# Optimization experiments

Measured on AMD Instinct MI355X. Metric: run time of the kernel, lower is better.

The kernel has to match this reference:

```python
import jax, jax.numpy as jnp
import numpy as np

V, D, F, H, NB, S, B = 16384, 512, 2048, 8, 4, 512, 2
T_STEPS = 3      # config.T: number of PC inference iterations
GAMMA = 0.1      # state-update step size


def _layernorm(x, s, b):
    m = x.mean(-1, keepdims=True)
    v = ((x - m) ** 2).mean(-1, keepdims=True)
    return (x - m) * jax.lax.rsqrt(v + 1e-5) * s + b


def setup_inputs() -> dict:
    key = jax.random.key(0)
    ks = jax.random.split(key, 12)
    r = lambda k, sh: jax.random.normal(k, sh, jnp.float32) * 0.02
    return {
        'word_emb': r(ks[0], (V, D)),
        'pos_emb': r(ks[1], (S, D)),
        'Wq': r(ks[2], (NB, D, D)),
        'Wk': r(ks[3], (NB, D, D)),
        'Wv': r(ks[4], (NB, D, D)),
        'bq': jnp.zeros((NB, D), jnp.float32),
        'bk': jnp.zeros((NB, D), jnp.float32),
        'bv': jnp.zeros((NB, D), jnp.float32),
        'Wo': r(ks[5], (NB, D, D)),
        'bo': jnp.zeros((NB, D), jnp.float32),
        'ln1_s': jnp.ones((NB, D), jnp.float32),
        'ln1_b': jnp.zeros((NB, D), jnp.float32),
        'ln2_s': jnp.ones((NB, D), jnp.float32),
        'ln2_b': jnp.zeros((NB, D), jnp.float32),
        'W1': r(ks[6], (NB, D, F)),
        'b1': jnp.zeros((NB, F), jnp.float32),
        'W2': r(ks[7], (NB, F, D)),
        'b2': jnp.zeros((NB, D), jnp.float32),
        'Wout': r(ks[8], (D, V)),
        'bout': jnp.zeros((V,), jnp.float32),
        'input_ids': jax.random.randint(ks[9], (B, S), 0, V),
        'target_ids': jax.random.randint(ks[10], (B, S), 0, V),
    }


def _forward(word_emb, pos_emb, Wq, Wk, Wv, bq, bk, bv, Wo, bo,
             ln1_s, ln1_b, ln2_s, ln2_b, W1, b1, W2, b2, Wout, bout,
             input_ids, target_ids):
    Bsz, Sl = input_ids.shape
    dh = D // H
    scale = 1.0 / float(np.sqrt(dh))
    ids = jnp.clip(input_ids, 0, V - 1)
    target = jax.nn.one_hot(jnp.clip(target_ids, 0, V - 1), V, dtype=word_emb.dtype)
    # bottom prediction: word + position embeddings
    mu_emb = word_emb[ids] + pos_emb[jnp.arange(Sl)][None]  # (B,S,D)
    causal = jnp.tril(jnp.ones((Sl, Sl), bool))
    neg = jnp.finfo(word_emb.dtype).min

    def attn(x, b):
        h = _layernorm(x, ln1_s[b], ln1_b[b])
        q = (h @ Wq[b] + bq[b]).reshape(Bsz, Sl, H, dh)
        k = (h @ Wk[b] + bk[b]).reshape(Bsz, Sl, H, dh)
        v = (h @ Wv[b] + bv[b]).reshape(Bsz, Sl, H, dh)
        sc = jnp.einsum('bqhd,bkhd->bhqk', q, k) * scale
        sc = jnp.where(causal, sc, neg)
        a = jax.nn.softmax(sc, axis=-1)
        return jnp.einsum('bhqk,bkhd->bqhd', a, v).reshape(Bsz, Sl, D)

    # generative functions g[l]: x_l -> mu_{l+1}; 4 PC layers per block
    # (pc_qkv->attn ctx, pc_output->Wo, pc_layer1->gelu(fc1), pc_layer2->fc2)
    gs = []
    for b in range(NB):
        gs.append(lambda x, b=b: attn(x, b))
        gs.append(lambda x, b=b: x @ Wo[b] + bo[b])
        gs.append(lambda x, b=b: jax.nn.gelu(_layernorm(x, ln2_s[b], ln2_b[b]) @ W1[b] + b1[b]))
        gs.append(lambda x, b=b: x @ W2[b] + b2[b])
    g_top = lambda x: x @ Wout + bout  # output pc layer -> logits mu

    # init_x: forward sweep sets each latent to its prediction
    xs = [mu_emb]
    for g in gs:
        xs.append(g(xs[-1]))
    L = len(gs)

    # T-step iterative PC inference: eps_l = x_l - mu_l, top clamped to target
    # x_l <- x_l + GAMMA * (J_{g_l}(x_l)^T eps_{l+1} - eps_l)
    for _ in range(T_STEPS):
        preds, vjps = [], []
        for l in range(L):
            mu, vj = jax.vjp(gs[l], xs[l])
            preds.append(mu)
            vjps.append(vj)
        logits, vj_top = jax.vjp(g_top, xs[L])
        eps = [xs[0] - mu_emb] + [xs[l + 1] - preds[l] for l in range(L)]
        eps_top = logits - target
        new_xs = []
        for l in range(L + 1):
            td = vjps[l](eps[l + 1])[0] if l < L else vj_top(eps_top)[0]
            new_xs.append(xs[l] + GAMMA * (td - eps[l]))
        xs = new_xs

    return g_top(xs[L])  # get_mu('linear_output')


def reference(word_emb, pos_emb, Wq, Wk, Wv, bq, bk, bv, Wo, bo,
              ln1_s, ln1_b, ln2_s, ln2_b, W1, b1, W2, b2, Wout, bout,
              input_ids, target_ids):
    return _forward(word_emb, pos_emb, Wq, Wk, Wv, bq, bk, bv, Wo, bo,
                    ln1_s, ln1_b, ln2_s, ln2_b, W1, b1, W2, b2, Wout, bout,
                    input_ids, target_ids)
```

## Files before the change

kernel.cpp:

```cpp
#include <hip/hip_runtime.h>
#include <hip/hip_bf16.h>
#include <math.h>

#define D_   512
#define F_   2048
#define V_   16384
#define H_   8
#define DH_  64
#define S_   512
#define B_   2
#define M_   1024
#define MD_  (M_ * D_)
#define MF_  (M_ * F_)
#define GAMMA_ 0.1f

typedef unsigned int u32;
typedef unsigned short u16;
typedef __attribute__((ext_vector_type(4))) float f32x4;
typedef __attribute__((ext_vector_type(8))) short s16x8;
typedef __attribute__((ext_vector_type(4))) u16 u16x4;
typedef __attribute__((ext_vector_type(8))) u16 u16x8;

__device__ __forceinline__ u16 f2b(float f) {
    __hip_bfloat16 h = __float2bfloat16(f);
    return *reinterpret_cast<u16*>(&h);
}
__device__ __forceinline__ float b2f(u16 v) {
    u32 u = ((u32)v) << 16;
    float f; __builtin_memcpy(&f, &u, 4); return f;
}
__device__ __forceinline__ u16x4 pack4(f32x4 v) {
    u16x4 o; o.x = f2b(v[0]); o.y = f2b(v[1]); o.z = f2b(v[2]); o.w = f2b(v[3]);
    return o;
}

__device__ __forceinline__ void gl_lds16(const void* g, void* l) {
    __builtin_amdgcn_global_load_lds((const __attribute__((address_space(1))) u32*)g,
                                     (__attribute__((address_space(3))) u32*)l, 16, 0, 0);
}

__device__ __forceinline__ float gelu_f(float v) {
    float u = 0.7978845608028654f * (v + 0.044715f * v * v * v);
    return 0.5f * v * (1.f + tanhf(u));
}

__device__ __forceinline__ f32x4 xpose4(f32x4 v, int b) {
#pragma unroll
    for (int s = 1; s < 4; s <<= 1) {
        f32x4 nv;
#pragma unroll
        for (int j = 0; j < 4; ++j) {
            float ex = __shfl_xor(v[j ^ s], s, 64);
            nv[j] = ((b ^ j) & s) ? ex : v[j];
        }
        v = nv;
    }
    return v;
}

__device__ __forceinline__ float wave_sum(float v) {
#pragma unroll
    for (int o = 32; o > 0; o >>= 1) v += __shfl_xor(v, o, 64);
    return v;
}

#define E_F32   0
#define E_GELU  1
#define E_TD    2
#define E_EC2   3
#define E_QKV3  4
#define E_OUT   5
#define E_BF16  6
#define E_SYM   7

template<int BK>
__device__ __forceinline__ int swz(int c, int row) {
    if constexpr (BK == 32) return c ^ ((row >> 1) & 3);
    else                    return c ^ (row & 7);
}

template<int BM, int BN, int BK, int FM, int FN, int EPI>
__global__ __launch_bounds__(256)
void mfma_gemm(const u16* __restrict__ A, const u16* __restrict__ B,
               float* __restrict__ Cf, u16* __restrict__ Cb,
               u16* __restrict__ Cb2, u16* __restrict__ Cb3,
               const float* __restrict__ bias,
               int K, int lda, int ldb, int ldc,
               long sC, long sKz, float alpha,
               const float* __restrict__ base, const float* __restrict__ subv,
               const float* __restrict__ cvec, const u16* __restrict__ woutTb,
               const int* __restrict__ tcl,
               float* __restrict__ ebF, u16* __restrict__ ebB)
{
    constexpr int WC = BN / (FN * 16);
    static_assert((BM / (FM * 16)) * WC == 4, "4 waves");
    constexpr int LPR = BK / 8;
    constexpr int RPI = 2048 / BK;
    constexpr int NISS = BM / RPI + BN / RPI;
    if constexpr (EPI == E_SYM) {
        if (blockIdx.x > blockIdx.y) return;
    }
    __shared__ __align__(16) u16 Asl[3][BM * BK];
    __shared__ __align__(16) u16 Bsl[3][BN * BK];
    const int t = threadIdx.x, l = t & 63, wid = t >> 6;
    const int m0 = blockIdx.y * BM, n0 = blockIdx.x * BN;
    const long z = blockIdx.z;
    A += z * sKz;
    B += z * sKz;
    if (Cf) Cf += z * sC;

    f32x4 acc[FM][FN] = {};
    const int rm = (wid / WC) * (FM * 16), cn = (wid % WC) * (FN * 16);
    const int lr = l & 15, hi = l >> 4;
    const int srl = t / LPR, sc = t % LPR;

    auto stage = [&](int k0, int pb) {
#pragma unroll
        for (int i = 0; i < BM / RPI; ++i) {
            int row = i * RPI + srl;
            gl_lds16(A + (size_t)(m0 + row) * lda + k0 + swz<BK>(sc, row) * 8,
                     &Asl[pb][i * 2048 + t * 8]);
        }
#pragma unroll
        for (int i = 0; i < BN / RPI; ++i) {
            int row = i * RPI + srl;
            gl_lds16(B + (size_t)(n0 + row) * ldb + k0 + swz<BK>(sc, row) * 8,
                     &Bsl[pb][i * 2048 + t * 8]);
        }
    };
    auto compute = [&](int pb) {
#pragma unroll
        for (int kk = 0; kk < BK / 32; ++kk) {
            s16x8 av[FM], bv[FN];
#pragma unroll
            for (int fm = 0; fm < FM; ++fm)
                av[fm] = *(const s16x8*)&Asl[pb][(rm + fm * 16 + lr) * BK + swz<BK>(kk * 4 + hi, lr) * 8];
#pragma unroll
            for (int fn = 0; fn < FN; ++fn)
                bv[fn] = *(const s16x8*)&Bsl[pb][(cn + fn * 16 + lr) * BK + swz<BK>(kk * 4 + hi, lr) * 8];
#pragma unroll
            for (int fm = 0; fm < FM; ++fm)
#pragma unroll
                for (int fn = 0; fn < FN; ++fn)
                    acc[fm][fn] = __builtin_amdgcn_mfma_f32_16x16x32_bf16(av[fm], bv[fn], acc[fm][fn], 0, 0, 0);
        }
    };

    const int nst = K / BK;
    stage(0, 0);
    if (nst > 1) stage(BK, 1);
    int rd = 0, wr = 2;
    for (int s = 0; s < nst; ++s) {
        if (s < nst - 1)
            asm volatile("s_waitcnt vmcnt(%0)" :: "i"(NISS) : "memory");
        else
            asm volatile("s_waitcnt vmcnt(0)" ::: "memory");
        __builtin_amdgcn_s_barrier();
        __builtin_amdgcn_sched_barrier(0);
        compute(rd);
        if (s + 2 < nst) stage((s + 2) * BK, wr);
        rd = (rd + 1 == 3) ? 0 : rd + 1;
        wr = (wr + 1 == 3) ? 0 : wr + 1;
    }

    const int qb = lr & 3, qi = lr >> 2;
#pragma unroll
    for (int fm = 0; fm < FM; ++fm)
#pragma unroll
        for (int fn = 0; fn < FN; ++fn) {
            const int gm = m0 + rm + fm * 16 + hi * 4 + qb;
            const int gn0 = n0 + cn + fn * 16 + qi * 4;
            const size_t idx0 = (size_t)gm * ldc + gn0;
            if constexpr (EPI == E_QKV3) {
                const int gnf = n0 + cn + fn * 16;
                const int sel = gnf >> 9;
                if (sel < 2) {
                    f32x4 v = xpose4(acc[fm][fn], qb);
                    f32x4 bv4 = *(const f32x4*)&bias[gn0];
#pragma unroll
                    for (int j = 0; j < 4; ++j) v[j] += bv4[j];
                    int b = gm >> 9, s = gm & (S_ - 1);
                    int d9 = gn0 & 511, h = d9 >> 6, d = d9 & 63;
                    u16* dst = (sel == 0) ? Cb : Cb2;
                    *(u16x4*)&dst[(((size_t)(b * H_ + h) * S_ + s) << 6) + d] = pack4(v);
                } else {
                    const int gnl = gnf + lr;
                    const int gm0 = m0 + rm + fm * 16 + hi * 4;
                    int b = gm0 >> 9, s0 = gm0 & (S_ - 1);
                    int d9 = gnl & 511, h = d9 >> 6, d = d9 & 63;
                    float bb = bias[gnl];
                    f32x4 v = acc[fm][fn];
#pragma unroll
                    for (int j = 0; j < 4; ++j) v[j] += bb;
                    *(u16x4*)&Cb3[((((size_t)(b * H_ + h)) << 6) + d) * S_ + s0] = pack4(v);
                }
            } else if constexpr (EPI == E_SYM) {
                const int gnr = n0 + cn + fn * 16 + lr;
                const int mc0 = m0 + rm + fm * 16 + hi * 4;
                *(f32x4*)&Cf[(size_t)gnr * ldc + mc0] = acc[fm][fn];
                f32x4 v = xpose4(acc[fm][fn], qb);
                *(f32x4*)&Cf[idx0] = v;
            } else {
                f32x4 v = xpose4(acc[fm][fn], qb);
                if constexpr (EPI == E_F32) {
#pragma unroll
                    for (int j = 0; j < 4; ++j) v[j] *= alpha;
                    if (bias) {
                        f32x4 bv4 = *(const f32x4*)&bias[gn0];
#pragma unroll
                        for (int j = 0; j < 4; ++j) v[j] += bv4[j];
                    }
                    *(f32x4*)&Cf[idx0] = v;
                    if (Cb) *(u16x4*)&Cb[idx0] = pack4(v);
                } else if constexpr (EPI == E_OUT) {
                    f32x4 bv4 = *(const f32x4*)&bias[gn0];
#pragma unroll
                    for (int j = 0; j < 4; ++j) v[j] += bv4[j];
                    *(f32x4*)&Cf[idx0] = v;
                } else if constexpr (EPI == E_GELU) {
                    f32x4 bv4 = *(const f32x4*)&bias[gn0];
#pragma unroll
                    for (int j = 0; j < 4; ++j) v[j] = gelu_f(v[j] + bv4[j]);
                    *(u16x4*)&Cb[idx0] = pack4(v);
                } else if constexpr (EPI == E_TD) {
                    const int tc = tcl[gm];
                    f32x4 cv4 = *(const f32x4*)&cvec[gn0];
                    f32x4 ba4 = *(const f32x4*)&base[idx0];
                    u16x4 gv = *(const u16x4*)&woutTb[(size_t)tc * D_ + gn0];
                    f32x4 dlt, o2;
#pragma unroll
                    for (int j = 0; j < 4; ++j)
                        dlt[j] = GAMMA_ * (v[j] + cv4[j] - b2f(gv[j]));
                    if (subv) {
                        f32x4 sv4 = *(const f32x4*)&subv[idx0];
#pragma unroll
                        for (int j = 0; j < 4; ++j) dlt[j] -= GAMMA_ * sv4[j];
                    }
#pragma unroll
                    for (int j = 0; j < 4; ++j) o2[j] = ba4[j] + dlt[j];
                    if (Cf) *(f32x4*)&Cf[idx0] = o2;
                    *(u16x4*)&Cb[idx0] = pack4(o2);
                    if (ebF) *(f32x4*)&ebF[idx0] = dlt;
                    if (ebB) *(u16x4*)&ebB[idx0] = pack4(dlt);
                } else if constexpr (EPI == E_EC2) {
                    f32x4 ba4 = *(const f32x4*)&base[idx0];
                    f32x4 sv4 = *(const f32x4*)&subv[idx0];
#pragma unroll
                    for (int j = 0; j < 4; ++j) v[j] = ba4[j] - sv4[j] - GAMMA_ * v[j];
                    *(f32x4*)&Cf[idx0] = v;
                } else if constexpr (EPI == E_BF16) {
                    *(u16x4*)&Cb[idx0] = pack4(v);
                }
            }
        }
}

__global__ __launch_bounds__(128)
void flash_attn(const u16* __restrict__ q, const u16* __restrict__ k,
                const u16* __restrict__ vT, u16* __restrict__ ctx)
{
    __shared__ __align__(16) u16 Ks[3][64 * 64];
    __shared__ __align__(16) u16 Vs[3][64 * 64];
    __shared__ __align__(16) u16 Ps[2][16 * 64];
    const int t = threadIdx.x, l = t & 63, w = t >> 6;
    const int qt = blockIdx.x, z = blockIdx.y;
    const int bb = z >> 3, hh = z & 7;
    const int lr = l & 15, hi = l >> 4;
    const u16* qp = q + (((size_t)z * S_ + qt * 32 + w * 16) << 6);
    const u16* kp = k + ((size_t)z * S_ << 6);
    const u16* vp = vT + (((size_t)z) << 6) * S_;

    const s16x8 aq0 = *(const s16x8*)&qp[lr * 64 + hi * 8];
    const s16x8 aq1 = *(const s16x8*)&qp[lr * 64 + 32 + hi * 8];

    f32x4 o[4] = {};
    float m[4], ls[4];
#pragma unroll
    for (int r = 0; r < 4; ++r) { m[r] = -3.0e38f; ls[r] = 0.f; }
    const int qrow = qt * 32 + w * 16 + hi * 4;
    const int srow = t >> 3, scl = t & 7;
    const int cg = (scl ^ (srow & 7)) * 8;
    const int sw7 = (lr & 7);
    const int jmax = qt >> 1;

    auto stage = [&](int j, int pb) {
#pragma unroll
        for (int i = 0; i < 4; ++i)
            gl_lds16(kp + ((size_t)(j * 64 + i * 16 + srow) << 6) + cg,
                     &Ks[pb][i * 1024 + t * 8]);
#pragma unroll
        for (int i = 0; i < 4; ++i)
            gl_lds16(vp + (size_t)(i * 16 + srow) * S_ + j * 64 + cg,
                     &Vs[pb][i * 1024 + t * 8]);
    };

    stage(0, 0);
    if (jmax > 0) stage(1, 1);
    int rd = 0, wr = 2;
    for (int j = 0; j <= jmax; ++j) {
        if (j < jmax) asm volatile("s_waitcnt vmcnt(8)" ::: "memory");
        else          asm volatile("s_waitcnt vmcnt(0)" ::: "memory");
        __builtin_amdgcn_s_barrier();
        __builtin_amdgcn_sched_barrier(0);

        float pv[4][4];
        __builtin_amdgcn_s_setprio(1);
#pragma unroll
        for (int fn = 0; fn < 4; ++fn) {
            f32x4 acc = {};
            acc = __builtin_amdgcn_mfma_f32_16x16x32_bf16(aq0,
                    *(const s16x8*)&Ks[rd][((fn * 16 + lr) << 6) + ((hi ^ sw7) * 8)], acc, 0, 0, 0);
            acc = __builtin_amdgcn_mfma_f32_16x16x32_bf16(aq1,
                    *(const s16x8*)&Ks[rd][((fn * 16 + lr) << 6) + (((hi + 4) ^ sw7) * 8)], acc, 0, 0, 0);
#pragma unroll
            for (int r = 0; r < 4; ++r) pv[fn][r] = acc[r] * 0.125f;
        }
        __builtin_amdgcn_s_setprio(0);
        if (j == jmax) {
#pragma unroll
            for (int fn = 0; fn < 4; ++fn) {
                int col = j * 64 + fn * 16 + lr;
#pragma unroll
                for (int r = 0; r < 4; ++r)
                    if (col > qrow + r) pv[fn][r] = -3.0e38f;
            }
        }
        float sc[4], rs[4];
#pragma unroll
        for (int r = 0; r < 4; ++r) {
            float x = fmaxf(fmaxf(pv[0][r], pv[1][r]), fmaxf(pv[2][r], pv[3][r]));
#pragma unroll
            for (int off = 1; off < 16; off <<= 1) x = fmaxf(x, __shfl_xor(x, off, 64));
            float nm = fmaxf(m[r], x);
            sc[r] = expf(m[r] - nm);
            m[r] = nm;
            rs[r] = 0.f;
        }
#pragma unroll
        for (int fn = 0; fn < 4; ++fn)
#pragma unroll
            for (int r = 0; r < 4; ++r) {
                float p = expf(pv[fn][r] - m[r]);
                pv[fn][r] = p;
                rs[r] += p;
            }
#pragma unroll
        for (int r = 0; r < 4; ++r) {
#pragma unroll
            for (int off = 1; off < 16; off <<= 1) rs[r] += __shfl_xor(rs[r], off, 64);
            ls[r] = ls[r] * sc[r] + rs[r];
        }
#pragma unroll
        for (int fn = 0; fn < 4; ++fn)
#pragma unroll
            for (int r = 0; r < 4; ++r) o[fn][r] *= sc[r];
#pragma unroll
        for (int fn = 0; fn < 4; ++fn)
#pragma unroll
            for (int r = 0; r < 4; ++r) {
                int qr = hi * 4 + r;
                int ci = (2 * fn + (lr >> 3)) ^ (qr & 7);
                Ps[w][qr * 64 + ci * 8 + (lr & 7)] = f2b(pv[fn][r]);
            }
        __builtin_amdgcn_s_setprio(1);
#pragma unroll
        for (int ks = 0; ks < 2; ++ks) {
            const s16x8 pa = *(const s16x8*)&Ps[w][lr * 64 + (((4 * ks + hi) ^ sw7) * 8)];
#pragma unroll
            for (int fn = 0; fn < 4; ++fn)
                o[fn] = __builtin_amdgcn_mfma_f32_16x16x32_bf16(pa,
                        *(const s16x8*)&Vs[rd][((fn * 16 + lr) << 6) + (((hi + 4 * ks) ^ sw7) * 8)], o[fn], 0, 0, 0);
        }
        __builtin_amdgcn_s_setprio(0);
        if (j + 2 <= jmax) stage(j + 2, wr);
        rd = (rd + 1 == 3) ? 0 : rd + 1;
        wr = (wr + 1 == 3) ? 0 : wr + 1;
    }
    float inv[4];
#pragma unroll
    for (int r = 0; r < 4; ++r) inv[r] = 1.f / ls[r];
    u16* cp = ctx + ((size_t)(bb * S_ + qt * 32 + w * 16) * D_) + hh * 64;
    const int qb = lr & 3, qi = lr >> 2;
#pragma unroll
    for (int fn = 0; fn < 4; ++fn) {
        f32x4 v = o[fn];
#pragma unroll
        for (int r = 0; r < 4; ++r) v[r] *= inv[r];
        v = xpose4(v, qb);
        *(u16x4*)&cp[(size_t)(hi * 4 + qb) * D_ + fn * 16 + qi * 4] = pack4(v);
    }
}

__global__ __launch_bounds__(256)
void mega_prep(const float* __restrict__ Wq, const float* __restrict__ Wk,
               const float* __restrict__ Wv, const float* __restrict__ Wo,
               const float* __restrict__ W1, const float* __restrict__ W2,
               const float* __restrict__ Wout,
               const float* __restrict__ bq, const float* __restrict__ bk,
               const float* __restrict__ bv, const int* __restrict__ target_ids,
               const float* __restrict__ we, const float* __restrict__ pe,
               const int* __restrict__ input_ids,
               const float* __restrict__ ln1s0, const float* __restrict__ ln1b0,
               u16* __restrict__ wqkvT, u16* __restrict__ woT, u16* __restrict__ w1T,
               u16* __restrict__ w2T, u16* __restrict__ woutT,
               u16* __restrict__ woutD, float* __restrict__ qkvb, int* __restrict__ tcl,
               u16* __restrict__ h_b)
{
    __shared__ float tile[64][65];
    __shared__ float sh2[4];
    const int g = blockIdx.x, t = threadIdx.x;

    if (g >= 1281) {
        const int rr = (g - 1281) * 2 + (t >> 7);
        const int lc = t & 127;
        const int ss = rr & (S_ - 1);
        int id = input_ids[rr];
        id = id < 0 ? 0 : (id > V_ - 1 ? V_ - 1 : id);
        const float4 a = ((const float4*)we)[(size_t)id * 128 + lc];
        const float4 b = ((const float4*)pe)[(size_t)ss * 128 + lc];
        float4 x;
        x.x = a.x + b.x; x.y = a.y + b.y; x.z = a.z + b.z; x.w = a.w + b.w;
        const int w = t >> 6, wb = (t >> 7) << 1;
        float s = wave_sum(x.x + x.y + x.z + x.w);
        if ((t & 63) == 0) sh2[w] = s;
        __syncthreads();
        float mu = (sh2[wb] + sh2[wb + 1]) * (1.f / D_);
        float d0 = x.x - mu, d1 = x.y - mu, d2 = x.z - mu, d3 = x.w - mu;
        float qv = wave_sum(d0 * d0 + d1 * d1 + d2 * d2 + d3 * d3);
        __syncthreads();
        if ((t & 63) == 0) sh2[w] = qv;
        __syncthreads();
        float var = (sh2[wb] + sh2[wb + 1]) * (1.f / D_);
        float r = rsqrtf(var + 1e-5f);
        const int c0 = lc * 4;
        float4 scv = *(const float4*)&ln1s0[c0];
        float4 bbv = *(const float4*)&ln1b0[c0];
        f32x4 o;
        o[0] = d0 * r * scv.x + bbv.x; o[1] = d1 * r * scv.y + bbv.y;
        o[2] = d2 * r * scv.z + bbv.z; o[3] = d3 * r * scv.w + bbv.w;
        *(u16x4*)&h_b[(size_t)rr * D_ + c0] = pack4(o);
        return;
    }
    if (g == 1280) {
        for (int i = t; i < M_; i += 256) {
            int v = target_ids[i];
            tcl[i] = v < 0 ? 0 : (v > V_ - 1 ? V_ - 1 : v);
        }
        for (int i = t; i < 4 * 1536; i += 256) {
            int b = i / 1536, j = i - b * 1536;
            qkvb[i] = (j < 512) ? bq[b * 512 + j]
                    : (j < 1024) ? bk[b * 512 + j - 512] : bv[b * 512 + j - 1024];
        }
        return;
    }

    const float* in = nullptr;
    u16 *outT = nullptr, *outC = nullptr;
    int R = 512, C = 512, c0 = 0, rbase = 0;

    if (g < 192) {
        int sel = g / 64, rem = g % 64, zz = rem >> 4, st = (rem >> 1) & 7, hf = rem & 1;
        in = (sel == 0 ? Wq : sel == 1 ? Wk : Wv) + (size_t)zz * 262144;
        outT = wqkvT + (size_t)zz * 786432 + sel * 262144;
        c0 = st * 64; rbase = hf * 256;
    } else if (g < 256) {
        int rem = g - 192, zz = rem >> 4, st = (rem >> 1) & 7, hf = rem & 1;
        in = Wo + (size_t)zz * 262144; outT = woT + (size_t)zz * 262144;
        c0 = st * 64; rbase = hf * 256;
    } else if (g < 512) {
        int rem = g - 256, zz = rem >> 6, sub = rem & 63, st = sub >> 1, hf = sub & 1;
        in = W1 + (size_t)zz * 1048576; outT = w1T + (size_t)zz * 1048576;
        C = 2048; c0 = st * 64; rbase = hf * 256;
    } else if (g < 768) {
        int rem = g - 512, zz = rem >> 6, sub = rem & 63, st = sub & 7, ch = sub >> 3;
        in = W2 + (size_t)zz * 1048576; outT = w2T + (size_t)zz * 1048576;
        R = 2048; c0 = st * 64; rbase = ch * 256;
    } else {
        int rem = g - 768, st = rem >> 1, hf = rem & 1;
        in = Wout; outT = woutT; outC = woutD;
        C = 16384; c0 = st * 64; rbase = hf * 256;
    }

    const int lrow = t >> 4, lcol = (t & 15) * 4;
    float4 va[2][4];
    auto loadit = [&](int it, int pb) {
#pragma unroll
        for (int p = 0; p < 4; ++p)
            va[pb][p] = *(const float4*)&in[(size_t)(rbase + it * 64 + p * 16 + lrow) * C + c0 + lcol];
    };

    loadit(0, 0);
#pragma unroll
    for (int it = 0; it < 4; ++it) {
        const int cur = it & 1;
        const int r0 = rbase + it * 64;
#pragma unroll
        for (int p = 0; p < 4; ++p) {
            float4 v = va[cur][p];
            int row = p * 16 + lrow;
            tile[row][lcol] = v.x; tile[row][lcol + 1] = v.y;
            tile[row][lcol + 2] = v.z; tile[row][lcol + 3] = v.w;
            if (outC) {
                f32x4 fv; fv[0] = v.x; fv[1] = v.y; fv[2] = v.z; fv[3] = v.w;
                *(u16x4*)&outC[(size_t)(r0 + row) * C + c0 + lcol] = pack4(fv);
            }
        }
        __syncthreads();
        if (it < 3) loadit(it + 1, cur ^ 1);
#pragma unroll
        for (int p = 0; p < 2; ++p) {
            int orow = p * 32 + (t >> 3), oc = (t & 7) * 8;
            u16x8 o;
#pragma unroll
            for (int j = 0; j < 8; ++j) o[j] = f2b(tile[oc + j][orow]);
            *(u16x8*)&outT[(size_t)(c0 + orow) * R + r0 + oc] = o;
        }
        __syncthreads();
    }
}

__global__ __launch_bounds__(256)
void gredcvec(const float* __restrict__ P, u16* __restrict__ G,
              const u16* __restrict__ woutD, const float* __restrict__ bout,
              float* __restrict__ cvec, const u16* __restrict__ w2T3,
              u16* __restrict__ H2)
{
    __shared__ __align__(16) u16 As2[2][32 * 64];
    __shared__ __align__(16) u16 Bs2[2][64 * 64];
    const int blk = blockIdx.x, t = threadIdx.x;
    if (blk < 1024) {
        int i = blk * 256 + t;
        float s = 0.f;
#pragma unroll
        for (int zz = 0; zz < 16; ++zz) s += P[(size_t)zz * D_ * D_ + i];
        G[i] = f2b(s);
    } else if (blk < 1152) {
        const int w = t >> 6, l = t & 63;
        const int d = (blk - 1024) * 4 + w;
        float s = 0.f;
        for (int it = 0; it < 32; ++it) {
            int base = it * 512 + l * 8;
            u16x8 wv = *(const u16x8*)&woutD[(size_t)d * V_ + base];
            float4 b0 = *(const float4*)&bout[base];
            float4 b1 = *(const float4*)&bout[base + 4];
            s += b2f(wv[0]) * b0.x + b2f(wv[1]) * b0.y + b2f(wv[2]) * b0.z + b2f(wv[3]) * b0.w
               + b2f(wv[4]) * b1.x + b2f(wv[5]) * b1.y + b2f(wv[6]) * b1.z + b2f(wv[7]) * b1.w;
        }
        s = wave_sum(s);
        if (l == 0) cvec[d] = s;
    } else {
        const int idx = blk - 1152;
        const int n0 = (idx & 7) * 64, m0 = (idx >> 3) * 32;
        const int l = t & 63, wid = t >> 6;
        const int lr = l & 15, hi = l >> 4;
        const int rm = (wid >> 1) * 16, cn = (wid & 1) * 32;
        const int srl = t >> 3, sc = t & 7;
        f32x4 acc2[2] = {};
        auto stg = [&](int k0, int pb) {
            gl_lds16(w2T3 + (size_t)(m0 + srl) * 2048 + k0 + swz<64>(sc, srl) * 8,
                     &As2[pb][t * 8]);
            gl_lds16(w2T3 + (size_t)(n0 + srl) * 2048 + k0 + swz<64>(sc, srl) * 8,
                     &Bs2[pb][t * 8]);
            gl_lds16(w2T3 + (size_t)(n0 + 32 + srl) * 2048 + k0 + swz<64>(sc, srl) * 8,
                     &Bs2[pb][2048 + t * 8]);
        };
        auto cmp = [&](int pb) {
#pragma unroll
            for (int kk = 0; kk < 2; ++kk) {
                s16x8 av = *(const s16x8*)&As2[pb][(rm + lr) * 64 + swz<64>(kk * 4 + hi, lr) * 8];
#pragma unroll
                for (int fn = 0; fn < 2; ++fn) {
                    s16x8 bv = *(const s16x8*)&Bs2[pb][(cn + fn * 16 + lr) * 64 + swz<64>(kk * 4 + hi, lr) * 8];
                    acc2[fn] = __builtin_amdgcn_mfma_f32_16x16x32_bf16(av, bv, acc2[fn], 0, 0, 0);
                }
            }
        };
        stg(0, 0);
        __syncthreads();
        int cur = 0;
        for (int k0 = 64; k0 < 2048; k0 += 64) {
            stg(k0, cur ^ 1);
            cmp(cur);
            __syncthreads();
            cur ^= 1;
        }
        cmp(cur);
        const int qb = lr & 3, qi = lr >> 2;
#pragma unroll
        for (int fn = 0; fn < 2; ++fn) {
            f32x4 v = xpose4(acc2[fn], qb);
            const int gm = m0 + rm + hi * 4 + qb;
            const int gn0 = n0 + cn + fn * 16 + qi * 4;
            *(u16x4*)&H2[(size_t)gm * D_ + gn0] = pack4(v);
        }
    }
}

__global__ __launch_bounds__(256)
void ln_fwd_kernel(const float* __restrict__ x, const float* __restrict__ s,
                   const float* __restrict__ bb, u16* __restrict__ h)
{
    const int l = threadIdx.x & 63, w = threadIdx.x >> 6;
    const int row = blockIdx.x * 4 + w;
    const float* xr = x + (size_t)row * D_;
    const int c0 = l * 8;
    float4 a = *(const float4*)&xr[c0];
    float4 b = *(const float4*)&xr[c0 + 4];
    float sum = a.x + a.y + a.z + a.w + b.x + b.y + b.z + b.w;
    float mu = wave_sum(sum) * (1.f / D_);
    float d0 = a.x - mu, d1 = a.y - mu, d2 = a.z - mu, d3 = a.w - mu;
    float d4 = b.x - mu, d5 = b.y - mu, d6 = b.z - mu, d7 = b.w - mu;
    float vs = d0*d0 + d1*d1 + d2*d2 + d3*d3 + d4*d4 + d5*d5 + d6*d6 + d7*d7;
    float var = wave_sum(vs) * (1.f / D_);
    float r = rsqrtf(var + 1e-5f);
    float4 s0 = *(const float4*)&s[c0], s1 = *(const float4*)&s[c0 + 4];
    float4 b0 = *(const float4*)&bb[c0], b1 = *(const float4*)&bb[c0 + 4];
    u16* hr = h + (size_t)row * D_;
    f32x4 o0, o1;
    o0[0] = d0 * r * s0.x + b0.x; o0[1] = d1 * r * s0.y + b0.y;
    o0[2] = d2 * r * s0.z + b0.z; o0[3] = d3 * r * s0.w + b0.w;
    o1[0] = d4 * r * s1.x + b1.x; o1[1] = d5 * r * s1.y + b1.y;
    o1[2] = d6 * r * s1.z + b1.z; o1[3] = d7 * r * s1.w + b1.w;
    *(u16x4*)&hr[c0] = pack4(o0);
    *(u16x4*)&hr[c0 + 4] = pack4(o1);
}

extern "C" void kernel_launch(void* const* d_in, const int* in_sizes, int n_in,
                              void* d_out, int out_size, void* d_ws, size_t ws_size,
                              hipStream_t stream)
{
    (void)in_sizes; (void)n_in; (void)out_size;
    const float* Wq  = (const float*)d_in[2];
    const float* Wk  = (const float*)d_in[3];
    const float* Wv  = (const float*)d_in[4];
    const float* bq  = (const float*)d_in[5];
    const float* bk  = (const float*)d_in[6];
    const float* bv  = (const float*)d_in[7];
    const float* Wo  = (const float*)d_in[8];
    const float* bo  = (const float*)d_in[9];
    const float* ln1_s = (const float*)d_in[10];
    const float* ln1_b = (const float*)d_in[11];
    const float* ln2_s = (const float*)d_in[12];
    const float* ln2_b = (const float*)d_in[13];
    const float* W1  = (const float*)d_in[14];
    const float* b1  = (const float*)d_in[15];
    const float* W2  = (const float*)d_in[16];
    const float* b2  = (const float*)d_in[17];
    const float* Wout = (const float*)d_in[18];
    const float* bout = (const float*)d_in[19];
    const int* input_ids  = (const int*)d_in[20];
    const int* target_ids = (const int*)d_in[21];
    float* out = (float*)d_out;

    char* wsb = (char*)d_ws;
    size_t off = 0;
    auto alloc = [&](size_t bytes) -> void* {
        off = (off + 255) & ~(size_t)255;
        void* p = wsb + off; off += bytes; return p;
    };
    u16* wqkvT = (u16*)alloc((size_t)4 * 1536 * D_ * 2);
    u16* woT   = (u16*)alloc((size_t)4 * D_ * D_ * 2);
    u16* w1T   = (u16*)alloc((size_t)4 * D_ * F_ * 2);
    u16* w2T   = (u16*)alloc((size_t)4 * D_ * F_ * 2);
    u16* woutT = (u16*)alloc((size_t)V_ * D_ * 2);
    u16* G_b   = (u16*)alloc((size_t)D_ * D_ * 2);
    u16* H2_b  = (u16*)alloc((size_t)D_ * D_ * 2);
    float* qkvb = (float*)alloc((size_t)4 * 1536 * 4);
    float* bufB = (float*)alloc((size_t)MD_ * 4);
    u16* h_b    = (u16*)alloc((size_t)MD_ * 2);
    u16* gelu_b = (u16*)alloc((size_t)MF_ * 2);
    u16* x16_b  = (u16*)alloc((size_t)MD_ * 2);
    float* cvec = (float*)alloc(D_ * 4);
    int* tcl    = (int*)alloc(M_ * 4);
    size_t uStart = (off + 255) & ~(size_t)255;
    off = uStart;
    u16* woutD   = (u16*)alloc((size_t)V_ * D_ * 2);
    float* Gpart = (float*)alloc((size_t)16 * D_ * D_ * 4);
    size_t endG = off;
    off = uStart;
    u16* q_b   = (u16*)alloc((size_t)MD_ * 2);
    u16* k_b   = (u16*)alloc((size_t)MD_ * 2);
    u16* v_b   = (u16*)alloc((size_t)MD_ * 2);
    u16* ctx_b = (u16*)alloc((size_t)MD_ * 2);
    size_t endA = off;
    off = uStart;
    float* xA  = (float*)alloc((size_t)MD_ * 4);
    float* xB  = (float*)alloc((size_t)MD_ * 4);
    float* eb  = (float*)alloc((size_t)MD_ * 4);
    float* ec  = (float*)alloc((size_t)MD_ * 4);
    u16* xA_b  = (u16*)alloc((size_t)MD_ * 2);
    u16* xB_b  = (u16*)alloc((size_t)MD_ * 2);
    u16* xC_b  = (u16*)alloc((size_t)MD_ * 2);
    u16* eb_b  = (u16*)alloc((size_t)MD_ * 2);
    size_t endT = off;
    size_t need = endG > endA ? endG : endA;
    if (endT > need) need = endT;
    if (need > ws_size) return;

    dim3 blk(256);
    const long NL = 0;
    #define GZ nullptr, nullptr, nullptr, nullptr, nullptr, nullptr, nullptr

    mega_prep<<<dim3(1793), blk, 0, stream>>>(Wq, Wk, Wv, Wo, W1, W2, Wout,
        bq, bk, bv, target_ids, (const float*)d_in[0], (const float*)d_in[1], input_ids,
        ln1_s, ln1_b, wqkvT, woT, w1T, w2T, woutT, woutD, qkvb, tcl, h_b);
    mfma_gemm<128, 128, 64, 4, 4, E_SYM><<<dim3(4, 4, 16), blk, 0, stream>>>(
        woutD, woutD, Gpart, nullptr, nullptr, nullptr, nullptr, 1024, V_, V_, D_,
        (long)D_ * D_, 1024, 1.f, GZ);
    gredcvec<<<dim3(1280), blk, 0, stream>>>(Gpart, G_b, woutD, bout, cvec,
        w2T + (size_t)3 * D_ * F_, H2_b);

    for (int b = 0; b < 4; ++b) {
        const size_t wDD = (size_t)b * D_ * D_, wDF = (size_t)b * D_ * F_;
        if (b)
            ln_fwd_kernel<<<dim3(M_ / 4), blk, 0, stream>>>(bufB, ln1_s + b * D_, ln1_b + b * D_, h_b);
        mfma_gemm<64, 64, 64, 2, 2, E_QKV3><<<dim3(24, 16, 1), blk, 0, stream>>>(
            h_b, wqkvT + (size_t)b * 1536 * 512, nullptr, q_b, k_b, v_b,
            qkvb + b * 1536, D_, D_, D_, 0, NL, NL, 1.f, GZ);
        flash_attn<<<dim3(16, 16), dim3(128), 0, stream>>>(q_b, k_b, v_b, ctx_b);
        mfma_gemm<32, 64, 64, 1, 2, E_F32><<<dim3(8, 32, 1), blk, 0, stream>>>(
            ctx_b, woT + wDD, bufB, nullptr, nullptr, nullptr, bo + b * D_,
            D_, D_, D_, D_, NL, NL, 1.f, GZ);
        ln_fwd_kernel<<<dim3(M_ / 4), blk, 0, stream>>>(bufB, ln2_s + b * D_, ln2_b + b * D_, h_b);
        mfma_gemm<64, 64, 64, 2, 2, E_GELU><<<dim3(32, 16, 1), blk, 0, stream>>>(
            h_b, w1T + wDF, nullptr, gelu_b, nullptr, nullptr, b1 + b * F_,
            D_, D_, D_, F_, NL, NL, 1.f, GZ);
        mfma_gemm<32, 64, 64, 1, 2, E_F32><<<dim3(8, 32, 1), blk, 0, stream>>>(
            gelu_b, w2T + wDF, bufB, (b == 3) ? x16_b : nullptr, nullptr, nullptr, b2 + b * D_,
            F_, F_, F_, D_, NL, NL, 1.f, GZ);
    }

    mfma_gemm<32, 64, 64, 1, 2, E_TD><<<dim3(8, 32, 1), blk, 0, stream>>>(
        x16_b, G_b, xA, xA_b, nullptr, nullptr, nullptr, D_, D_, D_, D_, NL, NL, 1.f,
        bufB, nullptr, cvec, woutT, tcl, eb, eb_b);
    mfma_gemm<32, 64, 64, 1, 2, E_TD><<<dim3(8, 32, 1), blk, 0, stream>>>(
        xA_b, G_b, xB, xB_b, nullptr, nullptr, nullptr, D_, D_, D_, D_, NL, NL, 1.f,
        xA, eb, cvec, woutT, tcl, nullptr, nullptr);
    mfma_gemm<32, 64, 64, 1, 2, E_EC2><<<dim3(8, 32, 1), blk, 0, stream>>>(
        eb_b, H2_b, ec, nullptr, nullptr, nullptr, nullptr, D_, D_, D_, D_, NL, NL, 1.f,
        xB, bufB, nullptr, nullptr, nullptr, nullptr, nullptr);
    mfma_gemm<32, 64, 64, 1, 2, E_TD><<<dim3(8, 32, 1), blk, 0, stream>>>(
        xB_b, G_b, nullptr, xC_b, nullptr, nullptr, nullptr, D_, D_, D_, D_, NL, NL, 1.f,
        xB, ec, cvec, woutT, tcl, nullptr, nullptr);
    mfma_gemm<128, 128, 32, 4, 4, E_OUT><<<dim3(128, 8, 1), blk, 0, stream>>>(
        xC_b, woutT, out, nullptr, nullptr, nullptr, bout, D_, D_, D_, V_, NL, NL, 1.f, GZ);
    #undef GZ
}
```

Baseline: 381.7 us.

## Fuse TD and EC2 GEMMs, pipeline weight transpose, halve Gram split-K

Adds a tdec kernel that runs the xA·G and eb·H2 GEMMs in one launch and computes both the xB state update and the ec error in a shared epilogue, replacing two separate GEMM launches. The weight-transpose prep now uses a three-slot register prefetch with a double-buffered LDS tile, which removes one barrier per iteration. The Gram-matrix split-K drops from 16 to 8 partitions, each with twice the K, so there are fewer partials to reduce but fewer blocks in flight. These changes trade less launch and memory traffic against lower parallelism in the Gram GEMM.

Measured after the change: 386.5 us (median of 2 runs). Within noise of the previous version (+1.3%).

```diff
diff --git a/kernel.cpp b/kernel.cpp
--- a/kernel.cpp
+++ b/kernel.cpp
@@ -67,11 +67,9 @@
 #define E_F32   0
 #define E_GELU  1
 #define E_TD    2
-#define E_EC2   3
-#define E_QKV3  4
-#define E_OUT   5
-#define E_BF16  6
-#define E_SYM   7
+#define E_QKV3  3
+#define E_OUT   4
+#define E_SYM   5
 
 template<int BK>
 __device__ __forceinline__ int swz(int c, int row) {
@@ -242,17 +240,97 @@
                     *(u16x4*)&Cb[idx0] = pack4(o2);
                     if (ebF) *(f32x4*)&ebF[idx0] = dlt;
                     if (ebB) *(u16x4*)&ebB[idx0] = pack4(dlt);
-                } else if constexpr (EPI == E_EC2) {
-                    f32x4 ba4 = *(const f32x4*)&base[idx0];
-                    f32x4 sv4 = *(const f32x4*)&subv[idx0];
-#pragma unroll
-                    for (int j = 0; j < 4; ++j) v[j] = ba4[j] - sv4[j] - GAMMA_ * v[j];
-                    *(f32x4*)&Cf[idx0] = v;
-                } else if constexpr (EPI == E_BF16) {
-                    *(u16x4*)&Cb[idx0] = pack4(v);
                 }
             }
         }
+}
+
+__global__ __launch_bounds__(256)
+void tdec_kernel(const u16* __restrict__ xAb, const u16* __restrict__ Gb,
+                 const u16* __restrict__ ebb, const u16* __restrict__ H2b,
+                 const float* __restrict__ xAf, const float* __restrict__ ebf,
+                 const float* __restrict__ x16f, const float* __restrict__ cvec,
+                 const u16* __restrict__ woutTb, const int* __restrict__ tcl,
+                 float* __restrict__ xBf, u16* __restrict__ xBb, float* __restrict__ ecf)
+{
+    constexpr int BM = 32, BN = 64, BK = 64;
+    __shared__ __align__(16) u16 Asl[3][BM * BK];
+    __shared__ __align__(16) u16 Bsl[3][BN * BK];
+    const int t = threadIdx.x, l = t & 63, wid = t >> 6;
+    const int m0 = blockIdx.y * BM, n0 = blockIdx.x * BN;
+    f32x4 a1[2] = {}, a2[2] = {};
+    const int rm = (wid >> 1) * 16, cn = (wid & 1) * 32;
+    const int lr = l & 15, hi = l >> 4;
+    const int srl = t >> 3, sc = t & 7;
+
+    auto stage = [&](int s, int pb) {
+        const u16* A = (s < 8) ? xAb : ebb;
+        const u16* B = (s < 8) ? Gb : H2b;
+        const int k0 = (s & 7) * BK;
+        {
+            int row = srl;
+            gl_lds16(A + (size_t)(m0 + row) * D_ + k0 + swz<64>(sc, row) * 8,
+                     &Asl[pb][t * 8]);
+        }
+#pragma unroll
+        for (int i = 0; i < 2; ++i) {
+            int row = i * 32 + srl;
+            gl_lds16(B + (size_t)(n0 + row) * D_ + k0 + swz<64>(sc, row) * 8,
+                     &Bsl[pb][i * 2048 + t * 8]);
+        }
+    };
+    auto cmp = [&](int pb, f32x4 (&ac)[2]) {
+#pragma unroll
+        for (int kk = 0; kk < 2; ++kk) {
+            s16x8 av = *(const s16x8*)&Asl[pb][(rm + lr) * BK + swz<64>(kk * 4 + hi, lr) * 8];
+#pragma unroll
+            for (int fn = 0; fn < 2; ++fn) {
+                s16x8 bv = *(const s16x8*)&Bsl[pb][(cn + fn * 16 + lr) * BK + swz<64>(kk * 4 + hi, lr) * 8];
+                ac[fn] = __builtin_amdgcn_mfma_f32_16x16x32_bf16(av, bv, ac[fn], 0, 0, 0);
+            }
+        }
+    };
+
+    stage(0, 0);
+    stage(1, 1);
+    int rd = 0, wr = 2;
+    for (int s = 0; s < 16; ++s) {
+        if (s < 15) asm volatile("s_waitcnt vmcnt(3)" ::: "memory");
+        else        asm volatile("s_waitcnt vmcnt(0)" ::: "memory");
+        __builtin_amdgcn_s_barrier();
+        __builtin_amdgcn_sched_barrier(0);
+        if (s < 8) cmp(rd, a1);
+        else       cmp(rd, a2);
+        if (s + 2 < 16) stage(s + 2, wr);
+        rd = (rd + 1 == 3) ? 0 : rd + 1;
+        wr = (wr + 1 == 3) ? 0 : wr + 1;
+    }
+
+    const int qb = lr & 3, qi = lr >> 2;
+#pragma unroll
+    for (int fn = 0; fn < 2; ++fn) {
+        f32x4 v1 = xpose4(a1[fn], qb);
+        f32x4 v2 = xpose4(a2[fn], qb);
+        const int gm = m0 + rm + hi * 4 + qb;
+        const int gn0 = n0 + cn + fn * 16 + qi * 4;
+        const size_t idx0 = (size_t)gm * D_ + gn0;
+        const int tc = tcl[gm];
+        f32x4 cv4 = *(const f32x4*)&cvec[gn0];
+        u16x4 gv = *(const u16x4*)&woutTb[(size_t)tc * D_ + gn0];
+        f32x4 xa4 = *(const f32x4*)&xAf[idx0];
+        f32x4 eb4 = *(const f32x4*)&ebf[idx0];
+        f32x4 x164 = *(const f32x4*)&x16f[idx0];
+        f32x4 xb4, ec4;
+#pragma unroll
+        for (int j = 0; j < 4; ++j) {
+            float dlt = GAMMA_ * (v1[j] + cv4[j] - b2f(gv[j]) - eb4[j]);
+            xb4[j] = xa4[j] + dlt;
+            ec4[j] = xb4[j] - x164[j] - GAMMA_ * v2[j];
+        }
+        *(f32x4*)&xBf[idx0] = xb4;
+        *(u16x4*)&xBb[idx0] = pack4(xb4);
+        *(f32x4*)&ecf[idx0] = ec4;
+    }
 }
 
 __global__ __launch_bounds__(128)
@@ -406,7 +484,7 @@
                u16* __restrict__ woutD, float* __restrict__ qkvb, int* __restrict__ tcl,
                u16* __restrict__ h_b)
 {
-    __shared__ float tile[64][65];
+    __shared__ float tile[2][64][65];
     __shared__ float sh2[4];
     const int g = blockIdx.x, t = threadIdx.x;
 
@@ -482,40 +560,41 @@
     }
 
     const int lrow = t >> 4, lcol = (t & 15) * 4;
-    float4 va[2][4];
-    auto loadit = [&](int it, int pb) {
+    float4 va[3][4];
+    auto loadit = [&](int it, int slot) {
 #pragma unroll
         for (int p = 0; p < 4; ++p)
-            va[pb][p] = *(const float4*)&in[(size_t)(rbase + it * 64 + p * 16 + lrow) * C + c0 + lcol];
+            va[slot][p] = *(const float4*)&in[(size_t)(rbase + it * 64 + p * 16 + lrow) * C + c0 + lcol];
     };
 
     loadit(0, 0);
+    loadit(1, 1);
 #pragma unroll
     for (int it = 0; it < 4; ++it) {
-        const int cur = it & 1;
+        const int slot = it % 3;
+        const int tb = it & 1;
         const int r0 = rbase + it * 64;
 #pragma unroll
         for (int p = 0; p < 4; ++p) {
-            float4 v = va[cur][p];
+            float4 v = va[slot][p];
             int row = p * 16 + lrow;
-            tile[row][lcol] = v.x; tile[row][lcol + 1] = v.y;
-            tile[row][lcol + 2] = v.z; tile[row][lcol + 3] = v.w;
+            tile[tb][row][lcol] = v.x; tile[tb][row][lcol + 1] = v.y;
+            tile[tb][row][lcol + 2] = v.z; tile[tb][row][lcol + 3] = v.w;
             if (outC) {
                 f32x4 fv; fv[0] = v.x; fv[1] = v.y; fv[2] = v.z; fv[3] = v.w;
                 *(u16x4*)&outC[(size_t)(r0 + row) * C + c0 + lcol] = pack4(fv);
             }
         }
+        if (it < 2) loadit(it + 2, (it + 2) % 3);
         __syncthreads();
-        if (it < 3) loadit(it + 1, cur ^ 1);
 #pragma unroll
         for (int p = 0; p < 2; ++p) {
             int orow = p * 32 + (t >> 3), oc = (t & 7) * 8;
             u16x8 o;
 #pragma unroll
-            for (int j = 0; j < 8; ++j) o[j] = f2b(tile[oc + j][orow]);
+            for (int j = 0; j < 8; ++j) o[j] = f2b(tile[tb][oc + j][orow]);
             *(u16x8*)&outT[(size_t)(c0 + orow) * R + r0 + oc] = o;
         }
-        __syncthreads();
     }
 }
 
@@ -532,7 +611,7 @@
         int i = blk * 256 + t;
         float s = 0.f;
 #pragma unroll
-        for (int zz = 0; zz < 16; ++zz) s += P[(size_t)zz * D_ * D_ + i];
+        for (int zz = 0; zz < 8; ++zz) s += P[(size_t)zz * D_ * D_ + i];
         G[i] = f2b(s);
     } else if (blk < 1152) {
         const int w = t >> 6, l = t & 63;
@@ -675,7 +754,7 @@
     size_t uStart = (off + 255) & ~(size_t)255;
     off = uStart;
     u16* woutD   = (u16*)alloc((size_t)V_ * D_ * 2);
-    float* Gpart = (float*)alloc((size_t)16 * D_ * D_ * 4);
+    float* Gpart = (float*)alloc((size_t)8 * D_ * D_ * 4);
     size_t endG = off;
     off = uStart;
     u16* q_b   = (u16*)alloc((size_t)MD_ * 2);
@@ -704,9 +783,9 @@
     mega_prep<<<dim3(1793), blk, 0, stream>>>(Wq, Wk, Wv, Wo, W1, W2, Wout,
         bq, bk, bv, target_ids, (const float*)d_in[0], (const float*)d_in[1], input_ids,
         ln1_s, ln1_b, wqkvT, woT, w1T, w2T, woutT, woutD, qkvb, tcl, h_b);
-    mfma_gemm<128, 128, 64, 4, 4, E_SYM><<<dim3(4, 4, 16), blk, 0, stream>>>(
-        woutD, woutD, Gpart, nullptr, nullptr, nullptr, nullptr, 1024, V_, V_, D_,
-        (long)D_ * D_, 1024, 1.f, GZ);
+    mfma_gemm<128, 128, 64, 4, 4, E_SYM><<<dim3(4, 4, 8), blk, 0, stream>>>(
+        woutD, woutD, Gpart, nullptr, nullptr, nullptr, nullptr, 2048, V_, V_, D_,
+        (long)D_ * D_, 2048, 1.f, GZ);
     gredcvec<<<dim3(1280), blk, 0, stream>>>(Gpart, G_b, woutD, bout, cvec,
         w2T + (size_t)3 * D_ * F_, H2_b);
 
@@ -733,12 +812,8 @@
     mfma_gemm<32, 64, 64, 1, 2, E_TD><<<dim3(8, 32, 1), blk, 0, stream>>>(
         x16_b, G_b, xA, xA_b, nullptr, nullptr, nullptr, D_, D_, D_, D_, NL, NL, 1.f,
         bufB, nullptr, cvec, woutT, tcl, eb, eb_b);
-    mfma_gemm<32, 64, 64, 1, 2, E_TD><<<dim3(8, 32, 1), blk, 0, stream>>>(
-        xA_b, G_b, xB, xB_b, nullptr, nullptr, nullptr, D_, D_, D_, D_, NL, NL, 1.f,
-        xA, eb, cvec, woutT, tcl, nullptr, nullptr);
-    mfma_gemm<32, 64, 64, 1, 2, E_EC2><<<dim3(8, 32, 1), blk, 0, stream>>>(
-        eb_b, H2_b, ec, nullptr, nullptr, nullptr, nullptr, D_, D_, D_, D_, NL, NL, 1.f,
-        xB, bufB, nullptr, nullptr, nullptr, nullptr, nullptr);
+    tdec_kernel<<<dim3(8, 32, 1), blk, 0, stream>>>(
+        xA_b, G_b, eb_b, H2_b, xA, eb, bufB, cvec, woutT, tcl, xB, xB_b, ec);
     mfma_gemm<32, 64, 64, 1, 2, E_TD><<<dim3(8, 32, 1), blk, 0, stream>>>(
         xB_b, G_b, nullptr, xC_b, nullptr, nullptr, nullptr, D_, D_, D_, D_, NL, NL, 1.f,
         xB, ec, cvec, woutT, tcl, nullptr, nullptr);
```
